# Kernel tuning notes

Measured on AMD Instinct MI355X. Metric: run time of the kernel, lower is better.

## Reference

```python
import jax, jax.numpy as jnp
import numpy as np

D_MODEL = 1024
NUM_HEADS = 16
D_K = D_MODEL // NUM_HEADS


def setup_inputs() -> dict:
    key = jax.random.key(0)
    ks = jax.random.split(key, 8)
    B, S = 2, 2048
    s = 1.0 / np.sqrt(D_MODEL)
    return {
        "query": jax.random.normal(ks[0], (B, S, D_MODEL), jnp.float32),
        "key": jax.random.normal(ks[1], (B, S, D_MODEL), jnp.float32),
        "value": jax.random.normal(ks[2], (B, S, D_MODEL), jnp.float32),
        "Wq": jax.random.normal(ks[3], (D_MODEL, D_MODEL), jnp.float32) * s,
        "bq": jnp.zeros((D_MODEL,), jnp.float32),
        "Wk": jax.random.normal(ks[4], (D_MODEL, D_MODEL), jnp.float32) * s,
        "bk": jnp.zeros((D_MODEL,), jnp.float32),
        "Wv": jax.random.normal(ks[5], (D_MODEL, D_K), jnp.float32) * s,
        "bv": jnp.zeros((D_K,), jnp.float32),
        "Wo": jax.random.normal(ks[6], (D_K, D_MODEL), jnp.float32) * (1.0 / np.sqrt(D_K)),
        "bo": jnp.zeros((D_MODEL,), jnp.float32),
    }


def reference(query, key, value, Wq, bq, Wk, bk, Wv, bv, Wo, bo):
    B, S, _ = query.shape
    scale = jnp.sqrt(jnp.asarray(D_K, query.dtype))
    # Per-head Q, K: [B, H, S, d_k]
    Q = (query @ Wq + bq).reshape(B, S, NUM_HEADS, D_K).transpose(0, 2, 1, 3)
    K = (key @ Wk + bk).reshape(B, -1, NUM_HEADS, D_K).transpose(0, 2, 1, 3)
    # Shared V across heads: [B, S, d_k]
    V = value @ Wv + bv
    scores = jnp.einsum("bhqd,bhkd->bhqk", Q, K) / scale
    attn = jax.nn.softmax(scores, axis=-1)
    avg_attn = attn.mean(axis=1)            # [B, S, S] head-averaged weights
    attn_output = jnp.einsum("bqk,bkd->bqd", avg_attn, V)
    output = attn_output @ Wo + bo
    return (output, avg_attn)
```

## Files before the change

kernel.cpp:

```cpp
#include <hip/hip_runtime.h>

#define BATCH 2
#define SEQ   2048
#define DMODEL 1024
#define NHEAD 16
#define DK    64
#define MROWS (BATCH * SEQ)
#define KSPLIT 4

using bf16x8 = __attribute__((ext_vector_type(8))) short;
using f32x4  = __attribute__((ext_vector_type(4))) float;

__device__ __forceinline__ unsigned short f2bf_rne(float x) {
    unsigned u = __float_as_uint(x);
    u += 0x7FFFu + ((u >> 16) & 1u);
    return (unsigned short)(u >> 16);
}
__device__ __forceinline__ float bf2f(unsigned short h) {
    return __uint_as_float((unsigned)h << 16);
}

__device__ __forceinline__ long long qf_addr(int row, int d) {
    const int qt = row >> 4, lid = row & 15;
    const int hh = d >> 6, ch = (d >> 3) & 7, j = d & 7;
    return ((((long long)qt * NHEAD + hh) * 8 + ch) * 16 + lid) * 8 + j;
}

__global__ __launch_bounds__(256) void conv_split_kernel(
    const float* __restrict__ x, unsigned short* __restrict__ hi,
    unsigned short* __restrict__ lo)
{
    const long long i = ((long long)blockIdx.x * 256 + threadIdx.x) * 4;
    float4 v = *(const float4*)&x[i];
    ushort4 h4, l4;
    unsigned short h;
    h = f2bf_rne(v.x); h4.x = h; l4.x = f2bf_rne(v.x - bf2f(h));
    h = f2bf_rne(v.y); h4.y = h; l4.y = f2bf_rne(v.y - bf2f(h));
    h = f2bf_rne(v.z); h4.z = h; l4.z = f2bf_rne(v.z - bf2f(h));
    h = f2bf_rne(v.w); h4.w = h; l4.w = f2bf_rne(v.w - bf2f(h));
    *(ushort4*)&hi[i] = h4;
    *(ushort4*)&lo[i] = l4;
}

__global__ __launch_bounds__(256) void conv_splitT_kernel(
    const float* __restrict__ W, unsigned short* __restrict__ hiT,
    unsigned short* __restrict__ loT)
{
    const int k0 = blockIdx.y * 64;
    const int n0 = blockIdx.x * 64;
    const int tid = threadIdx.x;
    __shared__ float T[64][68];
#pragma unroll
    for (int it = 0; it < 4; ++it) {
        const int r = it * 16 + (tid >> 4);
        const int c = (tid & 15) * 4;
        float4 v = *(const float4*)&W[(long long)(k0 + r) * DMODEL + n0 + c];
        T[r][c] = v.x; T[r][c + 1] = v.y; T[r][c + 2] = v.z; T[r][c + 3] = v.w;
    }
    __syncthreads();
#pragma unroll
    for (int it = 0; it < 4; ++it) {
        const int n = it * 16 + (tid >> 4);
        const int kc = (tid & 15) * 4;
        ushort4 h4, l4;
        float v; unsigned short h;
        v = T[kc + 0][n]; h = f2bf_rne(v); h4.x = h; l4.x = f2bf_rne(v - bf2f(h));
        v = T[kc + 1][n]; h = f2bf_rne(v); h4.y = h; l4.y = f2bf_rne(v - bf2f(h));
        v = T[kc + 2][n]; h = f2bf_rne(v); h4.z = h; l4.z = f2bf_rne(v - bf2f(h));
        v = T[kc + 3][n]; h = f2bf_rne(v); h4.w = h; l4.w = f2bf_rne(v - bf2f(h));
        const long long off = (long long)(n0 + n) * DMODEL + k0 + kc;
        *(ushort4*)&hiT[off] = h4;
        *(ushort4*)&loT[off] = l4;
    }
}

#define PA_HALF 8192
#define PA_TILE 16384
#define PB_HALF 4096
#define PB_TILE 8192

__global__ __launch_bounds__(256, 2) void proj_mfma_kernel(
    const unsigned short* __restrict__ AH, const unsigned short* __restrict__ AL,
    const unsigned short* __restrict__ BTH, const unsigned short* __restrict__ BTL,
    const float* __restrict__ bias,
    unsigned short* __restrict__ OH, unsigned short* __restrict__ OL, int fragQ)
{
    const int n0 = blockIdx.x * 64;
    const int m0 = blockIdx.y * 128;
    const int tid = threadIdx.x;
    const int w = tid >> 6, lane = tid & 63;
    const int quad = lane >> 4, lid = lane & 15;
    const int rsub = lane >> 3;
    const int slot = (lane & 7) ^ rsub;

    __shared__ unsigned short As[PA_TILE];
    __shared__ unsigned short Bs[PB_TILE];

    f32x4 acc[2][4] = {};

    for (int kc = 0; kc < DMODEL; kc += 64) {
        __syncthreads();
#pragma unroll
        for (int it = 0; it < 8; ++it) {
            const int c = it * 4 + w;
            const int half = c >> 4;
            const int row  = (c & 15) * 8 + rsub;
            const unsigned short* src = half ? AL : AH;
            const unsigned short* g = &src[(long long)(m0 + row) * DMODEL + kc + slot * 8];
            __builtin_amdgcn_global_load_lds(
                (const __attribute__((address_space(1))) unsigned int*)g,
                (__attribute__((address_space(3))) unsigned int*)(As + c * 512),
                16, 0, 0);
        }
#pragma unroll
        for (int it = 0; it < 4; ++it) {
            const int c = it * 4 + w;
            const int half = c >> 3;
            const int row  = (c & 7) * 8 + rsub;
            const unsigned short* src = half ? BTL : BTH;
            const unsigned short* g = &src[(long long)(n0 + row) * DMODEL + kc + slot * 8];
            __builtin_amdgcn_global_load_lds(
                (const __attribute__((address_space(1))) unsigned int*)g,
                (__attribute__((address_space(3))) unsigned int*)(Bs + c * 512),
                16, 0, 0);
        }
        __syncthreads();

#pragma unroll
        for (int ks = 0; ks < 2; ++ks) {
            bf16x8 ah[2], al_[2], bh[4], bl[4];
#pragma unroll
            for (int mt = 0; mt < 2; ++mt) {
                const int r = w * 32 + mt * 16 + lid;
                const int o = r * 64 + (((quad + 4 * ks) ^ (r & 7)) * 8);
                ah[mt]  = *(const bf16x8*)&As[o];
                al_[mt] = *(const bf16x8*)&As[PA_HALF + o];
            }
#pragma unroll
            for (int nt = 0; nt < 4; ++nt) {
                const int rn = nt * 16 + lid;
                const int o = rn * 64 + (((quad + 4 * ks) ^ (rn & 7)) * 8);
                bh[nt] = *(const bf16x8*)&Bs[o];
                bl[nt] = *(const bf16x8*)&Bs[PB_HALF + o];
            }
#pragma unroll
            for (int mt = 0; mt < 2; ++mt)
#pragma unroll
                for (int nt = 0; nt < 4; ++nt) {
                    acc[mt][nt] = __builtin_amdgcn_mfma_f32_16x16x32_bf16(ah[mt],  bh[nt], acc[mt][nt], 0, 0, 0);
                    acc[mt][nt] = __builtin_amdgcn_mfma_f32_16x16x32_bf16(ah[mt],  bl[nt], acc[mt][nt], 0, 0, 0);
                    acc[mt][nt] = __builtin_amdgcn_mfma_f32_16x16x32_bf16(al_[mt], bh[nt], acc[mt][nt], 0, 0, 0);
                }
        }
    }

    float bv[4];
#pragma unroll
    for (int nt = 0; nt < 4; ++nt)
        bv[nt] = bias[n0 + nt * 16 + lid];

#pragma unroll
    for (int mt = 0; mt < 2; ++mt)
#pragma unroll
        for (int nt = 0; nt < 4; ++nt) {
            const int col = n0 + nt * 16 + lid;
#pragma unroll
            for (int r = 0; r < 4; ++r) {
                const int row = m0 + w * 32 + mt * 16 + quad * 4 + r;
                const float val = acc[mt][nt][r] + bv[nt];
                const unsigned short h = f2bf_rne(val);
                const unsigned short l = f2bf_rne(val - bf2f(h));
                if (fragQ) {
                    const long long fa = qf_addr(row, col);
                    OH[fa] = h; OL[fa] = l;
                } else {
                    const long long off = (long long)row * DMODEL + col;
                    OH[off] = h; OL[off] = l;
                }
            }
        }
}

__global__ __launch_bounds__(256) void gemm_bias_kernel(
    const float* __restrict__ A, long long sA,
    const float* __restrict__ W, long long sW,
    const float* __restrict__ bias,
    float* __restrict__ C, long long sC,
    int M, int N, int K)
{
    A += (long long)blockIdx.z * sA;
    W += (long long)blockIdx.z * sW;
    C += (long long)blockIdx.z * sC;
    const int n0 = blockIdx.x * 64;
    const int m0 = blockIdx.y * 64;

    __shared__ float As[16][68];
    __shared__ float Bs[16][68];

    const int tid = threadIdx.x;
    const int tm = (tid >> 4) << 2;
    const int tn = (tid & 15) << 2;
    const int arow = tid >> 2, ak = (tid & 3) << 2;
    const int brow = tid >> 4, bn = (tid & 15) << 2;

    float acc[4][4] = {};

    for (int k0 = 0; k0 < K; k0 += 16) {
        float4 av = *(const float4*)&A[(long long)(m0 + arow) * K + k0 + ak];
        float4 wv = *(const float4*)&W[(long long)(k0 + brow) * N + n0 + bn];
        As[ak + 0][arow] = av.x;
        As[ak + 1][arow] = av.y;
        As[ak + 2][arow] = av.z;
        As[ak + 3][arow] = av.w;
        *(float4*)&Bs[brow][bn] = wv;
        __syncthreads();
#pragma unroll
        for (int kk = 0; kk < 16; ++kk) {
            float4 a4 = *(const float4*)&As[kk][tm];
            float4 b4 = *(const float4*)&Bs[kk][tn];
            float aa[4] = {a4.x, a4.y, a4.z, a4.w};
            float bb[4] = {b4.x, b4.y, b4.z, b4.w};
#pragma unroll
            for (int i = 0; i < 4; ++i)
#pragma unroll
                for (int j = 0; j < 4; ++j)
                    acc[i][j] = fmaf(aa[i], bb[j], acc[i][j]);
        }
        __syncthreads();
    }

    float4 bv = make_float4(0.f, 0.f, 0.f, 0.f);
    if (bias) bv = *(const float4*)&bias[n0 + tn];
#pragma unroll
    for (int i = 0; i < 4; ++i) {
        float4 o = make_float4(acc[i][0] + bv.x, acc[i][1] + bv.y,
                               acc[i][2] + bv.z, acc[i][3] + bv.w);
        *(float4*)&C[(long long)(m0 + tm + i) * N + n0 + tn] = o;
    }
}

__global__ __launch_bounds__(256) void gemm_splitk_kernel(
    const float* __restrict__ A, long long sA,
    const float* __restrict__ W, long long sW,
    float* __restrict__ P,
    int M, int N, int K, int nsplit)
{
    const int nbatch = gridDim.z / nsplit;
    const int b = blockIdx.z / nsplit;
    const int s = blockIdx.z % nsplit;
    A += (long long)b * sA;
    W += (long long)b * sW;
    float* Pout = P + ((long long)s * nbatch + b) * M * N;

    const int n0 = blockIdx.x * 64;
    const int m0 = blockIdx.y * 64;
    const int kb = s * (K / nsplit);
    const int kl = K / nsplit;

    __shared__ float As[16][68];
    __shared__ float Bs[16][68];

    const int tid = threadIdx.x;
    const int tm = (tid >> 4) << 2;
    const int tn = (tid & 15) << 2;
    const int arow = tid >> 2, ak = (tid & 3) << 2;
    const int brow = tid >> 4, bn = (tid & 15) << 2;

    float acc[4][4] = {};

    for (int k0 = 0; k0 < kl; k0 += 16) {
        float4 av = *(const float4*)&A[(long long)(m0 + arow) * K + kb + k0 + ak];
        float4 wv = *(const float4*)&W[(long long)(kb + k0 + brow) * N + n0 + bn];
        As[ak + 0][arow] = av.x;
        As[ak + 1][arow] = av.y;
        As[ak + 2][arow] = av.z;
        As[ak + 3][arow] = av.w;
        *(float4*)&Bs[brow][bn] = wv;
        __syncthreads();
#pragma unroll
        for (int kk = 0; kk < 16; ++kk) {
            float4 a4 = *(const float4*)&As[kk][tm];
            float4 b4 = *(const float4*)&Bs[kk][tn];
            float aa[4] = {a4.x, a4.y, a4.z, a4.w};
            float bb[4] = {b4.x, b4.y, b4.z, b4.w};
#pragma unroll
            for (int i = 0; i < 4; ++i)
#pragma unroll
                for (int j = 0; j < 4; ++j)
                    acc[i][j] = fmaf(aa[i], bb[j], acc[i][j]);
        }
        __syncthreads();
    }

#pragma unroll
    for (int i = 0; i < 4; ++i) {
        float4 o = make_float4(acc[i][0], acc[i][1], acc[i][2], acc[i][3]);
        *(float4*)&Pout[(long long)(m0 + tm + i) * N + n0 + tn] = o;
    }
}

__global__ __launch_bounds__(256) void reduce_bias_kernel(
    const float* __restrict__ P, const float* __restrict__ bias,
    float* __restrict__ C, long long stride, int nsplit, int N)
{
    const long long i = ((long long)blockIdx.x * 256 + threadIdx.x) * 4;
    float4 s = *(const float4*)&P[i];
    for (int k = 1; k < nsplit; ++k) {
        float4 v = *(const float4*)&P[(long long)k * stride + i];
        s.x += v.x; s.y += v.y; s.z += v.z; s.w += v.w;
    }
    if (bias) {
        const int n = (int)(i % N);
        float4 b4 = *(const float4*)&bias[n];
        s.x += b4.x; s.y += b4.y; s.z += b4.z; s.w += b4.w;
    }
    *(float4*)&C[i] = s;
}

#define HALF_USH 8192
#define TILE_USH 16384

__device__ __forceinline__ void stage_issue(
    const unsigned short* __restrict__ Khi, const unsigned short* __restrict__ Klo,
    unsigned short* KsBuf, long long grow0, int h, int w, int lane)
{
    const int rsub = lane >> 3;
    const int slot = (lane & 7) ^ rsub;
#pragma unroll
    for (int it = 0; it < 4; ++it) {
        const int c = it * 8 + w;
        const int half = c >> 4;
        const int row  = (c & 15) * 8 + rsub;
        const unsigned short* src = half ? Klo : Khi;
        const unsigned short* g = &src[(grow0 + row) * DMODEL + h * 64 + slot * 8];
        __builtin_amdgcn_global_load_lds(
            (const __attribute__((address_space(1))) unsigned int*)g,
            (__attribute__((address_space(3))) unsigned int*)(KsBuf + c * 512),
            16, 0, 0);
    }
}

__device__ __forceinline__ f32x4 mfma3(bf16x8 ah, bf16x8 al, bf16x8 bh, bf16x8 bl, f32x4 s) {
    s = __builtin_amdgcn_mfma_f32_16x16x32_bf16(ah, bh, s, 0, 0, 0);
    s = __builtin_amdgcn_mfma_f32_16x16x32_bf16(ah, bl, s, 0, 0, 0);
    s = __builtin_amdgcn_mfma_f32_16x16x32_bf16(al, bh, s, 0, 0, 0);
    return s;
}

__global__ __launch_bounds__(512, 4) void attn_stats_kernel(
    const unsigned short* __restrict__ QfH, const unsigned short* __restrict__ QfL,
    const unsigned short* __restrict__ Khi, const unsigned short* __restrict__ Klo,
    float* __restrict__ lsum)
{
    const int q0 = blockIdx.x * 256;
    const int h  = blockIdx.y;
    const int b  = blockIdx.z >> 2;
    const int kbase = (blockIdx.z & 3) * (SEQ / KSPLIT);
    const int tid = threadIdx.x;
    const int w = tid >> 6, lane = tid & 63;
    const int quad = lane >> 4, lid = lane & 15;

    __shared__ unsigned short Ks[2 * TILE_USH];

    bf16x8 ah[2][2], al[2][2];
#pragma unroll
    for (int mt = 0; mt < 2; ++mt) {
        const long long qt = (long long)(b * SEQ + q0) / 16 + w * 2 + mt;
#pragma unroll
        for (int ks = 0; ks < 2; ++ks) {
            const long long fa = (((qt * NHEAD + h) * 8 + (quad + 4 * ks)) * 16 + lid) * 8;
            ah[mt][ks] = *(const bf16x8*)&QfH[fa];
            al[mt][ks] = *(const bf16x8*)&QfL[fa];
        }
    }

    float ls[2][4] = {};
    const long long grow0 = (long long)b * SEQ + kbase;

    stage_issue(Khi, Klo, Ks, grow0, h, w, lane);
    __syncthreads();

    for (int kc = 0; kc < SEQ / KSPLIT; kc += 128) {
        const int buf = (kc >> 7) & 1;
        if (kc + 128 < SEQ / KSPLIT)
            stage_issue(Khi, Klo, Ks + (buf ^ 1) * TILE_USH,
                        grow0 + kc + 128, h, w, lane);
        const unsigned short* Kc = Ks + buf * TILE_USH;

#pragma unroll
        for (int kt = 0; kt < 8; ++kt) {
            const int rr = kt * 16 + lid;
            const int sw = rr & 7;
            bf16x8 bh[2], bl[2];
#pragma unroll
            for (int ks = 0; ks < 2; ++ks) {
                const int o = rr * 64 + (((quad + 4 * ks) ^ sw) * 8);
                bh[ks] = *(const bf16x8*)&Kc[o];
                bl[ks] = *(const bf16x8*)&Kc[HALF_USH + o];
            }
#pragma unroll
            for (int mt = 0; mt < 2; ++mt) {
                f32x4 s = {0.f, 0.f, 0.f, 0.f};
#pragma unroll
                for (int ks = 0; ks < 2; ++ks)
                    s = mfma3(ah[mt][ks], al[mt][ks], bh[ks], bl[ks], s);
#pragma unroll
                for (int r = 0; r < 4; ++r)
                    ls[mt][r] += __expf(s[r] * 0.125f);
            }
        }
        __syncthreads();
    }

#pragma unroll
    for (int off = 1; off < 16; off <<= 1)
#pragma unroll
        for (int mt = 0; mt < 2; ++mt)
#pragma unroll
            for (int r = 0; r < 4; ++r)
                ls[mt][r] += __shfl_xor(ls[mt][r], off);

    if (lid == 0) {
        const long long base = ((long long)(b * NHEAD + h)) * SEQ + q0 + w * 32 + quad * 4;
#pragma unroll
        for (int mt = 0; mt < 2; ++mt)
#pragma unroll
            for (int r = 0; r < 4; ++r)
                atomicAdd(&lsum[base + mt * 16 + r], ls[mt][r]);
    }
}

__global__ __launch_bounds__(256) void recip_kernel(float* __restrict__ p) {
    const int i = blockIdx.x * 256 + threadIdx.x;
    p[i] = 0.0625f / p[i];
}

__global__ __launch_bounds__(512, 4) void attn_avg_kernel(
    const unsigned short* __restrict__ QfH, const unsigned short* __restrict__ QfL,
    const unsigned short* __restrict__ Khi, const unsigned short* __restrict__ Klo,
    const float* __restrict__ cIn, float* __restrict__ avg)
{
    const int q0 = blockIdx.x * 128;
    const int k0 = blockIdx.y * 128;
    const int b  = blockIdx.z;
    const int tid = threadIdx.x;
    const int w = tid >> 6, lane = tid & 63;
    const int quad = lane >> 4, lid = lane & 15;

    __shared__ unsigned short Ks[2 * TILE_USH];

    f32x4 acc[8] = {};
    const long long grow0 = (long long)b * SEQ + k0;
    const long long qt = (long long)(b * SEQ + q0) / 16 + w;

    stage_issue(Khi, Klo, Ks, grow0, 0, w, lane);
    __syncthreads();

    for (int h = 0; h < NHEAD; ++h) {
        bf16x8 ah[2], al[2];
        float c_[4];
#pragma unroll
        for (int ks = 0; ks < 2; ++ks) {
            const long long fa = (((qt * NHEAD + h) * 8 + (quad + 4 * ks)) * 16 + lid) * 8;
            ah[ks] = *(const bf16x8*)&QfH[fa];
            al[ks] = *(const bf16x8*)&QfL[fa];
        }
        const long long cb = ((long long)(b * NHEAD + h)) * SEQ + q0 + w * 16 + quad * 4;
#pragma unroll
        for (int r = 0; r < 4; ++r)
            c_[r] = cIn[cb + r];

        const int buf = h & 1;
        if (h + 1 < NHEAD)
            stage_issue(Khi, Klo, Ks + (buf ^ 1) * TILE_USH,
                        grow0, h + 1, w, lane);
        const unsigned short* Kc = Ks + buf * TILE_USH;

#pragma unroll
        for (int kt = 0; kt < 8; ++kt) {
            const int rr = kt * 16 + lid;
            const int sw = rr & 7;
            bf16x8 bh[2], bl[2];
#pragma unroll
            for (int ks = 0; ks < 2; ++ks) {
                const int o = rr * 64 + (((quad + 4 * ks) ^ sw) * 8);
                bh[ks] = *(const bf16x8*)&Kc[o];
                bl[ks] = *(const bf16x8*)&Kc[HALF_USH + o];
            }
            f32x4 s = {0.f, 0.f, 0.f, 0.f};
#pragma unroll
            for (int ks = 0; ks < 2; ++ks)
                s = mfma3(ah[ks], al[ks], bh[ks], bl[ks], s);
#pragma unroll
            for (int r = 0; r < 4; ++r)
                acc[kt][r] = fmaf(__expf(s[r] * 0.125f), c_[r], acc[kt][r]);
        }
        __syncthreads();
    }

#pragma unroll
    for (int kt = 0; kt < 8; ++kt)
#pragma unroll
        for (int r = 0; r < 4; ++r) {
            const int q = q0 + w * 16 + quad * 4 + r;
            avg[((long long)(b * SEQ + q)) * SEQ + k0 + kt * 16 + lid] = acc[kt][r];
        }
}

extern "C" void kernel_launch(void* const* d_in, const int* in_sizes, int n_in,
                              void* d_out, int out_size, void* d_ws, size_t ws_size,
                              hipStream_t stream)
{
    const float* query = (const float*)d_in[0];
    const float* key   = (const float*)d_in[1];
    const float* value = (const float*)d_in[2];
    const float* Wq    = (const float*)d_in[3];
    const float* bq    = (const float*)d_in[4];
    const float* Wk    = (const float*)d_in[5];
    const float* bk    = (const float*)d_in[6];
    const float* Wv    = (const float*)d_in[7];
    const float* bv    = (const float*)d_in[8];
    const float* Wo    = (const float*)d_in[9];
    const float* bo    = (const float*)d_in[10];

    float* out = (float*)d_out;
    float* avg = out + (long long)BATCH * SEQ * DMODEL;

    const long long QKN = (long long)MROWS * DMODEL;
    unsigned short* QfH = (unsigned short*)d_ws;
    unsigned short* QfL = QfH + QKN;
    unsigned short* Khi = QfL + QKN;
    unsigned short* Klo = Khi + QKN;
    unsigned short* AspH = Klo + QKN;
    unsigned short* AspL = AspH + QKN;
    unsigned short* WTh  = AspL + QKN;
    unsigned short* WTl  = WTh + (long long)DMODEL * DMODEL;
    float* Vb   = (float*)(WTl + (long long)DMODEL * DMODEL);
    float* lBuf = Vb + (long long)MROWS * DK;
    float* ao   = lBuf + (long long)BATCH * NHEAD * SEQ;

    float* Pv  = (float*)AspH;
    float* Pav = (float*)QfH;

    dim3 blk(256);
    hipMemsetAsync(lBuf, 0, (size_t)BATCH * NHEAD * SEQ * sizeof(float), stream);

    const int convGrid = (int)(QKN / (256 * 4));
    dim3 tGrid(DMODEL / 64, DMODEL / 64);
    dim3 pGrid(DMODEL / 64, MROWS / 128);

    conv_split_kernel<<<convGrid, blk, 0, stream>>>(query, AspH, AspL);
    conv_splitT_kernel<<<tGrid, blk, 0, stream>>>(Wq, WTh, WTl);
    proj_mfma_kernel<<<pGrid, blk, 0, stream>>>(AspH, AspL, WTh, WTl, bq, QfH, QfL, 1);

    conv_split_kernel<<<convGrid, blk, 0, stream>>>(key, AspH, AspL);
    conv_splitT_kernel<<<tGrid, blk, 0, stream>>>(Wk, WTh, WTl);
    proj_mfma_kernel<<<pGrid, blk, 0, stream>>>(AspH, AspL, WTh, WTl, bk, Khi, Klo, 0);

    gemm_splitk_kernel<<<dim3(DK / 64, MROWS / 64, 16), blk, 0, stream>>>(
        value, 0, Wv, 0, Pv, MROWS, DK, DMODEL, 16);
    reduce_bias_kernel<<<dim3((int)((long long)MROWS * DK / 1024)), blk, 0, stream>>>(
        Pv, bv, Vb, (long long)MROWS * DK, 16, DK);

    attn_stats_kernel<<<dim3(SEQ / 256, NHEAD, BATCH * KSPLIT), dim3(512), 0, stream>>>(
        QfH, QfL, Khi, Klo, lBuf);
    recip_kernel<<<dim3(BATCH * NHEAD * SEQ / 256), blk, 0, stream>>>(lBuf);

    attn_avg_kernel<<<dim3(SEQ / 128, SEQ / 128, BATCH), dim3(512), 0, stream>>>(
        QfH, QfL, Khi, Klo, lBuf, avg);

    gemm_splitk_kernel<<<dim3(DK / 64, SEQ / 64, BATCH * 32), blk, 0, stream>>>(
        avg, (long long)SEQ * SEQ, Vb, (long long)SEQ * DK, Pav, SEQ, DK, SEQ, 32);
    reduce_bias_kernel<<<dim3((int)((long long)MROWS * DK / 1024)), blk, 0, stream>>>(
        Pav, nullptr, ao, (long long)MROWS * DK, 32, DK);

    gemm_bias_kernel<<<dim3(DMODEL / 64, MROWS / 64, 1), blk, 0, stream>>>(
        ao, 0, Wo, 0, bo, out, 0, MROWS, DMODEL, DK);
}
```

Measured before the change: 359.1 us.

## Remap attention blocks for XCD locality, prefetch Q, fuse reciprocal, raise MFMA priority

Both attention kernels now remap the linear block id so that consecutive blocks on the same XCD share K or Q tiles, aiming for better L2 reuse. The avg kernel loads the next head's Q fragments and normaliser coefficients one iteration early to hide global-load latency. It also computes 1/lsum in place, which removes the separate recip kernel launch. s_setprio is raised around the MFMA chains to favour matrix issue. The trade-off is extra registers for the prefetched fragments, which could lower occupancy.

```diff
diff --git a/kernel.cpp b/kernel.cpp
--- a/kernel.cpp
+++ b/kernel.cpp
@@ -352,10 +352,13 @@
     const unsigned short* __restrict__ Khi, const unsigned short* __restrict__ Klo,
     float* __restrict__ lsum)
 {
-    const int q0 = blockIdx.x * 256;
-    const int h  = blockIdx.y;
-    const int b  = blockIdx.z >> 2;
-    const int kbase = (blockIdx.z & 3) * (SEQ / KSPLIT);
+    int lin = blockIdx.x + 8 * (blockIdx.y + 16 * blockIdx.z);
+    lin = (lin & 7) * 128 + (lin >> 3);
+    const int q0 = (lin & 7) * 256;
+    const int h  = (lin >> 3) & 15;
+    const int zz = lin >> 7;
+    const int b  = zz >> 2;
+    const int kbase = (zz & 3) * (SEQ / KSPLIT);
     const int tid = threadIdx.x;
     const int w = tid >> 6, lane = tid & 63;
     const int quad = lane >> 4, lid = lane & 15;
@@ -401,9 +404,11 @@
 #pragma unroll
             for (int mt = 0; mt < 2; ++mt) {
                 f32x4 s = {0.f, 0.f, 0.f, 0.f};
+                __builtin_amdgcn_s_setprio(1);
 #pragma unroll
                 for (int ks = 0; ks < 2; ++ks)
                     s = mfma3(ah[mt][ks], al[mt][ks], bh[ks], bl[ks], s);
+                __builtin_amdgcn_s_setprio(0);
 #pragma unroll
                 for (int r = 0; r < 4; ++r)
                     ls[mt][r] += __expf(s[r] * 0.125f);
@@ -430,19 +435,16 @@
     }
 }
 
-__global__ __launch_bounds__(256) void recip_kernel(float* __restrict__ p) {
-    const int i = blockIdx.x * 256 + threadIdx.x;
-    p[i] = 0.0625f / p[i];
-}
-
 __global__ __launch_bounds__(512, 4) void attn_avg_kernel(
     const unsigned short* __restrict__ QfH, const unsigned short* __restrict__ QfL,
     const unsigned short* __restrict__ Khi, const unsigned short* __restrict__ Klo,
-    const float* __restrict__ cIn, float* __restrict__ avg)
-{
-    const int q0 = blockIdx.x * 128;
-    const int k0 = blockIdx.y * 128;
-    const int b  = blockIdx.z;
+    const float* __restrict__ lsum, float* __restrict__ avg)
+{
+    int lin = blockIdx.x + 16 * (blockIdx.y + 16 * blockIdx.z);
+    lin = (lin & 7) * 64 + (lin >> 3);
+    const int q0 = (lin & 15) * 128;
+    const int k0 = ((lin >> 4) & 15) * 128;
+    const int b  = lin >> 8;
     const int tid = threadIdx.x;
     const int w = tid >> 6, lane = tid & 63;
     const int quad = lane >> 4, lid = lane & 15;
@@ -452,28 +454,43 @@
     f32x4 acc[8] = {};
     const long long grow0 = (long long)b * SEQ + k0;
     const long long qt = (long long)(b * SEQ + q0) / 16 + w;
+    const long long cb0 = ((long long)b * NHEAD) * SEQ + q0 + w * 16 + quad * 4;
+
+    bf16x8 ahC[2], alC[2];
+    float cC[4];
+#pragma unroll
+    for (int ks = 0; ks < 2; ++ks) {
+        const long long fa = (((qt * NHEAD + 0) * 8 + (quad + 4 * ks)) * 16 + lid) * 8;
+        ahC[ks] = *(const bf16x8*)&QfH[fa];
+        alC[ks] = *(const bf16x8*)&QfL[fa];
+    }
+#pragma unroll
+    for (int r = 0; r < 4; ++r)
+        cC[r] = 0.0625f / lsum[cb0 + r];
 
     stage_issue(Khi, Klo, Ks, grow0, 0, w, lane);
     __syncthreads();
 
     for (int h = 0; h < NHEAD; ++h) {
-        bf16x8 ah[2], al[2];
-        float c_[4];
-#pragma unroll
-        for (int ks = 0; ks < 2; ++ks) {
-            const long long fa = (((qt * NHEAD + h) * 8 + (quad + 4 * ks)) * 16 + lid) * 8;
-            ah[ks] = *(const bf16x8*)&QfH[fa];
-            al[ks] = *(const bf16x8*)&QfL[fa];
-        }
-        const long long cb = ((long long)(b * NHEAD + h)) * SEQ + q0 + w * 16 + quad * 4;
-#pragma unroll
-        for (int r = 0; r < 4; ++r)
-            c_[r] = cIn[cb + r];
-
         const int buf = h & 1;
         if (h + 1 < NHEAD)
             stage_issue(Khi, Klo, Ks + (buf ^ 1) * TILE_USH,
                         grow0, h + 1, w, lane);
+
+        bf16x8 ahN[2], alN[2];
+        float cN[4];
+        if (h + 1 < NHEAD) {
+#pragma unroll
+            for (int ks = 0; ks < 2; ++ks) {
+                const long long fa = (((qt * NHEAD + (h + 1)) * 8 + (quad + 4 * ks)) * 16 + lid) * 8;
+                ahN[ks] = *(const bf16x8*)&QfH[fa];
+                alN[ks] = *(const bf16x8*)&QfL[fa];
+            }
+#pragma unroll
+            for (int r = 0; r < 4; ++r)
+                cN[r] = 0.0625f / lsum[cb0 + (long long)(h + 1) * SEQ + r];
+        }
+
         const unsigned short* Kc = Ks + buf * TILE_USH;
 
 #pragma unroll
@@ -488,14 +505,23 @@
                 bl[ks] = *(const bf16x8*)&Kc[HALF_USH + o];
             }
             f32x4 s = {0.f, 0.f, 0.f, 0.f};
+            __builtin_amdgcn_s_setprio(1);
 #pragma unroll
             for (int ks = 0; ks < 2; ++ks)
-                s = mfma3(ah[ks], al[ks], bh[ks], bl[ks], s);
+                s = mfma3(ahC[ks], alC[ks], bh[ks], bl[ks], s);
+            __builtin_amdgcn_s_setprio(0);
 #pragma unroll
             for (int r = 0; r < 4; ++r)
-                acc[kt][r] = fmaf(__expf(s[r] * 0.125f), c_[r], acc[kt][r]);
-        }
-        __syncthreads();
+                acc[kt][r] = fmaf(__expf(s[r] * 0.125f), cC[r], acc[kt][r]);
+        }
+        __syncthreads();
+
+        if (h + 1 < NHEAD) {
+#pragma unroll
+            for (int ks = 0; ks < 2; ++ks) { ahC[ks] = ahN[ks]; alC[ks] = alN[ks]; }
+#pragma unroll
+            for (int r = 0; r < 4; ++r) cC[r] = cN[r];
+        }
     }
 
 #pragma unroll
@@ -564,7 +590,6 @@
 
     attn_stats_kernel<<<dim3(SEQ / 256, NHEAD, BATCH * KSPLIT), dim3(512), 0, stream>>>(
         QfH, QfL, Khi, Klo, lBuf);
-    recip_kernel<<<dim3(BATCH * NHEAD * SEQ / 256), blk, 0, stream>>>(lBuf);
 
     attn_avg_kernel<<<dim3(SEQ / 128, SEQ / 128, BATCH), dim3(512), 0, stream>>>(
         QfH, QfL, Khi, Klo, lBuf, avg);
```

After: 357.6 us. No clear change (-0.4%).
